# Performance work log

Hardware: AMD Instinct MI355X
Metric: run time of the kernel (lower is better)

## Reference

```python
import jax, jax.numpy as jnp
import numpy as np

WS = 4        # window_size
HEADS = 12    # num_heads


def setup_inputs() -> dict:
    key = jax.random.key(0)
    k1, k2, k3 = jax.random.split(key, 3)
    B, N, E = 32, 4096, 384
    x = jax.random.normal(k1, (B, N, E), dtype=jnp.float32)
    w_in = jax.random.normal(k2, (3 * E, E), dtype=jnp.float32) * 0.02
    b_in = jnp.zeros((3 * E,), dtype=jnp.float32)
    w_out = jax.random.normal(k3, (E, E), dtype=jnp.float32) * 0.02
    b_out = jnp.zeros((E,), dtype=jnp.float32)
    return {"x": x, "w_in": w_in, "b_in": b_in, "w_out": w_out, "b_out": b_out}


def reference(x, w_in, b_in, w_out, b_out):
    B, N, E = x.shape
    H = W = int(np.sqrt(N))
    nh, nw = H // WS, W // WS
    hd = E // HEADS
    T = WS * WS  # tokens per window

    # window partition: [B, H, W, E] -> [B*nh*nw, T, E]
    xw = x.reshape(B, nh, WS, nw, WS, E)
    xw = xw.transpose(0, 1, 3, 2, 4, 5).reshape(-1, T, E)

    # packed QKV projection (torch nn.MultiheadAttention in_proj)
    qkv = xw @ w_in.T + b_in                      # [nWin, T, 3E]
    q, k, v = jnp.split(qkv, 3, axis=-1)          # each [nWin, T, E]

    def split_heads(t):
        return t.reshape(-1, T, HEADS, hd).transpose(0, 2, 1, 3)  # [nWin, h, T, hd]

    q, k, v = split_heads(q), split_heads(k), split_heads(v)
    scale = 1.0 / np.sqrt(hd).astype(np.float32)
    scores = jnp.einsum('whqd,whkd->whqk', q * scale, k)          # [nWin, h, T, T]
    attn = jax.nn.softmax(scores, axis=-1)
    out = jnp.einsum('whqk,whkd->whqd', attn, v)                  # [nWin, h, T, hd]
    out = out.transpose(0, 2, 1, 3).reshape(-1, T, E)
    out = out @ w_out.T + b_out                                   # out_proj

    # window reverse: [B*nh*nw, T, E] -> [B, N, E]
    out = out.reshape(B, nh, nw, WS, WS, E)
    out = out.transpose(0, 1, 3, 2, 4, 5).reshape(B, N, E)
    return out
```

## Files before the change

kernel.cpp:

```cpp
#include <hip/hip_runtime.h>
#include <hip/hip_bf16.h>

typedef __attribute__((ext_vector_type(8))) short short8;
typedef __attribute__((ext_vector_type(4))) float f32x4;

static __device__ __forceinline__ f32x4 MFMA16(short8 a, short8 b, f32x4 c) {
    return __builtin_amdgcn_mfma_f32_16x16x32_bf16(a, b, c, 0, 0, 0);
}
static __device__ __forceinline__ unsigned short f2bf(float f) {
    union { __hip_bfloat16 h; unsigned short u; } c;
    c.h = __float2bfloat16(f);
    return c.u;
}
static __device__ __forceinline__ void gload16(const void* g, void* l) {
    __builtin_amdgcn_global_load_lds(
        (const __attribute__((address_space(1))) unsigned int*)g,
        (__attribute__((address_space(3))) unsigned int*)l, 16, 0, 0);
}

constexpr size_t kWstOff = 0;
constexpr size_t kWosOff = 884736;
constexpr size_t kBrrOff = 1179648;
constexpr size_t kAttOff = 1184256;

__global__ void prep(const float* __restrict__ w_in, const float* __restrict__ b_in,
                     const float* __restrict__ w_out,
                     char* __restrict__ wst, char* __restrict__ wos,
                     float* __restrict__ brr)
{
    const int i = blockIdx.x * 256 + threadIdx.x;
    if (i < 55296) {
        int h = i / 4608, rem = i % 4608;
        int s = rem / 768, t = rem % 768;
        int row = t >> 3, sl = t & 7;
        int c8 = sl ^ (row & 7);
        int sec = row >> 5, d = row & 31;
        int srow = sec * 384 + h * 32 + d;
        int k0 = s * 64 + c8 * 8;
        const float4* src = (const float4*)(w_in + (size_t)srow * 384 + k0);
        float4 a = src[0], b = src[1];
        uint4 w;
        w.x = f2bf(a.x) | ((unsigned)f2bf(a.y) << 16);
        w.y = f2bf(a.z) | ((unsigned)f2bf(a.w) << 16);
        w.z = f2bf(b.x) | ((unsigned)f2bf(b.y) << 16);
        w.w = f2bf(b.z) | ((unsigned)f2bf(b.w) << 16);
        *(uint4*)(wst + (size_t)i * 16) = w;
    } else {
        int j = i - 55296;
        int nb = j / 6144, rem = j % 6144;
        int s = rem / 1024, slot16 = rem % 1024;
        int row = slot16 >> 3, sl = slot16 & 7;
        int c8 = sl ^ (row & 7);
        int srow = nb * 128 + row;
        int k0 = s * 64 + c8 * 8;
        const float4* src = (const float4*)(w_out + (size_t)srow * 384 + k0);
        float4 a = src[0], b = src[1];
        uint4 w;
        w.x = f2bf(a.x) | ((unsigned)f2bf(a.y) << 16);
        w.y = f2bf(a.z) | ((unsigned)f2bf(a.w) << 16);
        w.z = f2bf(b.x) | ((unsigned)f2bf(b.y) << 16);
        w.w = f2bf(b.z) | ((unsigned)f2bf(b.w) << 16);
        *(uint4*)(wos + (size_t)j * 16) = w;
    }
    if (i < 1152) {
        int h = i / 96, jj = i % 96;
        int sec = jj >> 5, d = jj & 31;
        brr[i] = b_in[sec * 384 + h * 32 + d];
    }
}

__global__ void prep_x(const float* __restrict__ x, char* __restrict__ xbf)
{
    const int i = blockIdx.x * 256 + threadIdx.x;
    const int lane = i & 63;
    const int cc = (i >> 6) & 1;
    const int f = (i >> 7) & 7;
    const int rem = i >> 10;
    const int s = rem % 6, mb = rem / 6;

    int T = mb * 128 + f * 16 + (lane & 15);
    int win = T >> 4, t4 = T & 15;
    int bb = win >> 8, wh = (win >> 4) & 15, ww = win & 15;
    int n = (wh * 4 + (t4 >> 2)) * 64 + ww * 4 + (t4 & 3);
    int k0 = s * 64 + cc * 32 + (lane >> 4) * 8;

    const float4* src = (const float4*)(x + ((size_t)bb * 4096 + n) * 384 + k0);
    float4 a = src[0], b = src[1];
    uint4 w;
    w.x = f2bf(a.x) | ((unsigned)f2bf(a.y) << 16);
    w.y = f2bf(a.z) | ((unsigned)f2bf(a.w) << 16);
    w.z = f2bf(b.x) | ((unsigned)f2bf(b.y) << 16);
    w.w = f2bf(b.z) | ((unsigned)f2bf(b.w) << 16);
    *(uint4*)(xbf + (size_t)i * 16) = w;
}

__global__ __launch_bounds__(512, 6)
void qkv_attn(const char* __restrict__ xbf, const char* __restrict__ wst,
              const float* __restrict__ brr, char* __restrict__ attst)
{
    __shared__ __align__(16) char smem[49152];

    const int tid  = threadIdx.x;
    const int lane = tid & 63, wid = tid >> 6;
    const int g = lane >> 4, r16 = lane & 15;

    int b = blockIdx.x;
    int x8 = b & 7, j = b >> 3;
    const int head = j % 12;
    const int mblk = x8 * 128 + j / 12;

    const char* xw = xbf + (size_t)mblk * 98304 + (size_t)wid * 2048 + lane * 16;
    const char* whp = wst + (size_t)head * 73728;

    auto stage_B = [&](int s, int buf) {
        char* dst = smem + buf * 12288;
        const char* src = whp + s * 12288;
        gload16(src + tid * 16, dst + tid * 16);
        if (tid < 256) gload16(src + 8192 + tid * 16, dst + 8192 + tid * 16);
    };

    f32x4 acc[6] = {};

    stage_B(0, 0);
    for (int s = 0; s < 6; ++s) {
        __syncthreads();
        short8 a[2];
        a[0] = *(const short8*)(xw + s * 16384);
        a[1] = *(const short8*)(xw + s * 16384 + 1024);
        __builtin_amdgcn_sched_barrier(0);
        if (s < 5) stage_B(s + 1, (s + 1) & 1);

        const char* bbp = smem + (s & 1) * 12288;
        #pragma unroll
        for (int c = 0; c < 2; ++c) {
            const int sw = ((c * 4 + g) ^ (r16 & 7)) << 4;
            #pragma unroll
            for (int nh = 0; nh < 2; ++nh) {
                short8 bf[3];
                #pragma unroll
                for (int k = 0; k < 3; ++k)
                    bf[k] = *(const short8*)(bbp + ((nh * 3 + k) * 16 + r16) * 128 + sw);
                #pragma unroll
                for (int k = 0; k < 3; ++k)
                    acc[nh * 3 + k] = MFMA16(a[c], bf[k], acc[nh * 3 + k]);
            }
        }
    }

    char* tile = smem + 24576 + wid * 3072;
    #pragma unroll
    for (int ni = 0; ni < 6; ++ni) {
        const int sec = ni >> 1;
        const int d = (ni & 1) * 16 + r16;
        const float bias = brr[head * 96 + ni * 16 + r16];
        float v0 = acc[ni][0] + bias;
        float v1 = acc[ni][1] + bias;
        float v2 = acc[ni][2] + bias;
        float v3 = acc[ni][3] + bias;
        uint2 w;
        w.x = f2bf(v0) | ((unsigned)f2bf(v1) << 16);
        w.y = f2bf(v2) | ((unsigned)f2bf(v3) << 16);
        *(uint2*)(tile + sec * 1024 + d * 32 + g * 8) = w;
    }

    const float kC = 0.17677669529663687f * 1.4426950408889634f;
    const f32x4 zero = {0.f, 0.f, 0.f, 0.f};

    union U8 { unsigned short e[8]; short8 v; };
    U8 ku, qu;
    #pragma unroll
    for (int jj = 0; jj < 8; ++jj) {
        const int off = (g * 8 + jj) * 32 + r16 * 2;
        qu.e[jj] = *(const unsigned short*)(tile + off);
        ku.e[jj] = *(const unsigned short*)(tile + 1024 + off);
    }
    f32x4 s = MFMA16(ku.v, qu.v, zero);

    float m = fmaxf(fmaxf(s[0], s[1]), fmaxf(s[2], s[3]));
    m = fmaxf(m, __shfl_xor(m, 16, 64));
    m = fmaxf(m, __shfl_xor(m, 32, 64));
    float p[4], sum = 0.f;
    #pragma unroll
    for (int r = 0; r < 4; ++r) { p[r] = exp2f((s[r] - m) * kC); sum += p[r]; }
    sum += __shfl_xor(sum, 16, 64);
    sum += __shfl_xor(sum, 32, 64);
    const float inv = 1.f / sum;

    U8 pu;
    pu.e[0] = f2bf(p[0] * inv); pu.e[1] = f2bf(p[1] * inv);
    pu.e[2] = f2bf(p[2] * inv); pu.e[3] = f2bf(p[3] * inv);
    pu.e[4] = 0; pu.e[5] = 0; pu.e[6] = 0; pu.e[7] = 0;

    f32x4 o[2];
    #pragma unroll
    for (int ti = 0; ti < 2; ++ti) {
        U8 vu;
        *(uint2*)&vu.e[0] = *(const uint2*)(tile + 2048 + (ti * 16 + r16) * 32 + g * 8);
        vu.e[4] = 0; vu.e[5] = 0; vu.e[6] = 0; vu.e[7] = 0;
        o[ti] = MFMA16(pu.v, vu.v, zero);
    }

    #pragma unroll
    for (int ti = 0; ti < 2; ++ti)
        #pragma unroll
        for (int r = 0; r < 4; ++r)
            *(unsigned short*)(tile + (g * 4 + r) * 64 + (ti * 16 + r16) * 2)
                = f2bf(o[ti][r]);
    uint4 ov = *(const uint4*)(tile + r16 * 64 + g * 16);

    int row7 = wid * 16 + r16;
    int col8 = head * 4 + g;
    int sst = col8 >> 3;
    int sl = (col8 & 7) ^ (row7 & 7);
    *(uint4*)(attst + (size_t)mblk * 98304 + sst * 16384 + row7 * 128 + sl * 16) = ov;
}

__global__ __launch_bounds__(256, 2)
void out_proj(const char* __restrict__ attst, const char* __restrict__ wos,
              const float* __restrict__ b_out, float* __restrict__ out)
{
    __shared__ __align__(16) char smem[65536];

    const int tid  = threadIdx.x;
    const int lane = tid & 63, wid = tid >> 6;
    const int g = lane >> 4, r16 = lane & 15;
    const int wm = wid >> 1, wn = wid & 1;

    int b = blockIdx.x;
    int L = (b & 7) * 384 + (b >> 3);
    const int mblk = L / 3, nblk = L - mblk * 3;

    auto stage = [&](int s, int buf) {
        const char* asrc = attst + (size_t)mblk * 98304 + s * 16384 + wid * 4096 + lane * 16;
        const char* bsrc = wos   + (size_t)nblk * 98304 + s * 16384 + wid * 4096 + lane * 16;
        char* adst = smem + buf * 16384 + wid * 4096;
        char* bdst = smem + 32768 + buf * 16384 + wid * 4096;
        #pragma unroll
        for (int j = 0; j < 4; ++j) {
            gload16(asrc + j * 1024, adst + j * 1024);
            gload16(bsrc + j * 1024, bdst + j * 1024);
        }
    };

    f32x4 acc[4][4] = {};
    auto compute = [&](int buf) {
        const char* ab = smem + buf * 16384;
        const char* bbp = smem + 32768 + buf * 16384;
        #pragma unroll
        for (int c = 0; c < 2; ++c) {
            const int sw = ((c * 4 + g) ^ (r16 & 7)) << 4;
            short8 a[4], bf[4];
            #pragma unroll
            for (int mi = 0; mi < 4; ++mi)
                a[mi] = *(const short8*)(ab + (wm * 64 + mi * 16 + r16) * 128 + sw);
            #pragma unroll
            for (int ni = 0; ni < 4; ++ni)
                bf[ni] = *(const short8*)(bbp + (wn * 64 + ni * 16 + r16) * 128 + sw);
            #pragma unroll
            for (int mi = 0; mi < 4; ++mi)
                #pragma unroll
                for (int ni = 0; ni < 4; ++ni)
                    acc[mi][ni] = MFMA16(a[mi], bf[ni], acc[mi][ni]);
        }
    };

    stage(0, 0);
    for (int s = 0; s < 6; ++s) {
        __syncthreads();
        if (s < 5) stage(s + 1, (s + 1) & 1);
        compute(s & 1);
    }

    float bias[4];
    #pragma unroll
    for (int ni = 0; ni < 4; ++ni) bias[ni] = b_out[nblk * 128 + wn * 64 + ni * 16 + r16];

    #pragma unroll
    for (int mi = 0; mi < 4; ++mi) {
        #pragma unroll
        for (int r = 0; r < 4; ++r) {
            int T = mblk * 128 + wm * 64 + mi * 16 + g * 4 + r;
            int win = T >> 4, tt = T & 15;
            int bb = win >> 8, wh = (win >> 4) & 15, ww = win & 15;
            size_t o = ((size_t)bb * 4096 + (wh * 4 + (tt >> 2)) * 64 + ww * 4 + (tt & 3)) * 384
                     + nblk * 128 + wn * 64;
            #pragma unroll
            for (int ni = 0; ni < 4; ++ni)
                out[o + ni * 16 + r16] = acc[mi][ni][r] + bias[ni];
        }
    }
}

extern "C" void kernel_launch(void* const* d_in, const int* in_sizes, int n_in,
                              void* d_out, int out_size, void* d_ws, size_t ws_size,
                              hipStream_t stream) {
    const float* x     = (const float*)d_in[0];
    const float* w_in  = (const float*)d_in[1];
    const float* b_in  = (const float*)d_in[2];
    const float* w_out = (const float*)d_in[3];
    const float* b_out = (const float*)d_in[4];
    float* out = (float*)d_out;

    char* ws = (char*)d_ws;
    char*  wst = ws + kWstOff;
    char*  wos = ws + kWosOff;
    float* brr = (float*)(ws + kBrrOff);
    char*  att = ws + kAttOff;
    char*  xbf = (char*)d_out;

    prep<<<dim3(288), dim3(256), 0, stream>>>(w_in, b_in, w_out, wst, wos, brr);
    prep_x<<<dim3(24576), dim3(256), 0, stream>>>(x, xbf);
    qkv_attn<<<dim3(12288), dim3(512), 0, stream>>>(xbf, wst, brr, att);
    out_proj<<<dim3(3072), dim3(256), 0, stream>>>(att, wos, b_out, out);
}
```

Baseline: 274.8 us.

## Triple-buffer weight staging and prefetch activation fragments one step ahead

The QKV GEMM loop in qkv_attn moves from double to triple buffering of the weight tiles in LDS, issuing loads two stages ahead. It replaces __syncthreads with explicit vmcnt waits plus s_barrier, and prefetches the next step's x fragments into registers. The epilogue tile now reuses the staging buffers, which shrinks shared memory from 48KB to 36KB and could allow more resident blocks. The aim is to hide global-load latency behind the MFMAs. The cost is more register pressure and hand-managed waitcnt logic, which is fragile.

```diff
diff --git a/kernel.cpp b/kernel.cpp
--- a/kernel.cpp
+++ b/kernel.cpp
@@ -98,7 +98,7 @@
 void qkv_attn(const char* __restrict__ xbf, const char* __restrict__ wst,
               const float* __restrict__ brr, char* __restrict__ attst)
 {
-    __shared__ __align__(16) char smem[49152];
+    __shared__ __align__(16) char smem[36864];
 
     const int tid  = threadIdx.x;
     const int lane = tid & 63, wid = tid >> 6;
@@ -113,27 +113,45 @@
     const char* whp = wst + (size_t)head * 73728;
 
     auto stage_B = [&](int s, int buf) {
-        char* dst = smem + buf * 12288;
-        const char* src = whp + s * 12288;
-        gload16(src + tid * 16, dst + tid * 16);
-        if (tid < 256) gload16(src + 8192 + tid * 16, dst + 8192 + tid * 16);
+        if (tid < 384) {
+            char* dst = smem + buf * 12288 + tid * 16;
+            const char* src = whp + s * 12288 + tid * 16;
+            gload16(src, dst);
+            gload16(src + 6144, dst + 6144);
+        }
     };
 
     f32x4 acc[6] = {};
+    short8 acur0, acur1, anext0, anext1;
 
     stage_B(0, 0);
+    acur0 = *(const short8*)(xw);
+    acur1 = *(const short8*)(xw + 1024);
+    stage_B(1, 1);
+
+    #pragma unroll
     for (int s = 0; s < 6; ++s) {
-        __syncthreads();
-        short8 a[2];
-        a[0] = *(const short8*)(xw + s * 16384);
-        a[1] = *(const short8*)(xw + s * 16384 + 1024);
         __builtin_amdgcn_sched_barrier(0);
-        if (s < 5) stage_B(s + 1, (s + 1) & 1);
-
-        const char* bbp = smem + (s & 1) * 12288;
+        if (s < 5 && wid < 6) {
+            asm volatile("s_waitcnt vmcnt(2)" ::: "memory");
+        } else {
+            asm volatile("s_waitcnt vmcnt(0)" ::: "memory");
+        }
+        __builtin_amdgcn_sched_barrier(0);
+        __builtin_amdgcn_s_barrier();
+        __builtin_amdgcn_sched_barrier(0);
+
+        if (s < 5) {
+            anext0 = *(const short8*)(xw + (s + 1) * 16384);
+            anext1 = *(const short8*)(xw + (s + 1) * 16384 + 1024);
+        }
+        if (s < 4) stage_B(s + 2, (s + 2) % 3);
+
+        const char* bbp = smem + (s % 3) * 12288;
         #pragma unroll
         for (int c = 0; c < 2; ++c) {
             const int sw = ((c * 4 + g) ^ (r16 & 7)) << 4;
+            const short8 ac = (c == 0) ? acur0 : acur1;
             #pragma unroll
             for (int nh = 0; nh < 2; ++nh) {
                 short8 bf[3];
@@ -142,12 +160,14 @@
                     bf[k] = *(const short8*)(bbp + ((nh * 3 + k) * 16 + r16) * 128 + sw);
                 #pragma unroll
                 for (int k = 0; k < 3; ++k)
-                    acc[nh * 3 + k] = MFMA16(a[c], bf[k], acc[nh * 3 + k]);
+                    acc[nh * 3 + k] = MFMA16(ac, bf[k], acc[nh * 3 + k]);
             }
         }
-    }
-
-    char* tile = smem + 24576 + wid * 3072;
+        acur0 = anext0;
+        acur1 = anext1;
+    }
+
+    char* tile = smem + wid * 3072;
     #pragma unroll
     for (int ni = 0; ni < 6; ++ni) {
         const int sec = ni >> 1;
```

Result: no change. 272.9 us (-0.7%).
